# Performance work log

Measured on AMD Instinct MI355X. Metric: run time of the kernel, lower is better.

## Reference

```python
import jax, jax.numpy as jnp
import numpy as np

QMAX = 127.0  # 2**(8-1) - 1 for n_bits=8

def fake_quant_last_dim(t):
    # per-row absmax fake quant over last dim (per-token for acts, per-channel for weights)
    scales = jnp.max(jnp.abs(t), axis=-1, keepdims=True)
    scales = jnp.clip(scales, 1e-05, None) / QMAX
    return jnp.round(t / scales) * scales

def setup_inputs() -> dict:
    key = jax.random.key(0)
    k1, k2, k3 = jax.random.split(key, 3)
    B, S, D_in, D_out = 4, 2048, 4096, 4096
    return {
        "input": jax.random.normal(k1, (B, S, D_in), dtype=jnp.float32),
        "weight": jax.random.normal(k2, (D_out, D_in), dtype=jnp.float32) * 0.02,
        "bias": jax.random.normal(k3, (D_out,), dtype=jnp.float32) * 0.02,
    }

def reference(input, weight, bias):
    w_q = fake_quant_last_dim(weight)          # per-output-channel
    x_q = fake_quant_last_dim(input)           # per-token
    y = jnp.einsum('bsi,oi->bso', x_q, w_q) + bias
    return fake_quant_last_dim(y)              # per-token output quant
```

## Files before the change

### kernel.cpp

```cpp
#include <hip/hip_runtime.h>

typedef unsigned int u32;
typedef __attribute__((ext_vector_type(4))) int i32x4;

#define BM 256
#define BN 256
#define BKT 64

__device__ __forceinline__ void gload16(const void* g, void* l) {
  __builtin_amdgcn_global_load_lds(
      (const __attribute__((address_space(1))) unsigned int*)g,
      (__attribute__((address_space(3))) unsigned int*)l, 16, 0, 0);
}

__device__ __forceinline__ u32 pack4_i8(float4 v, float scale) {
  const int a = (int)rintf(v.x / scale);
  const int b = (int)rintf(v.y / scale);
  const int c = (int)rintf(v.z / scale);
  const int d = (int)rintf(v.w / scale);
  return (u32)(a & 255) | (((u32)(b & 255)) << 8) |
         (((u32)(c & 255)) << 16) | (((u32)(d & 255)) << 24);
}

__global__ __launch_bounds__(256) void quant_rows4096_kernel(
    const float* __restrict__ src, u32* __restrict__ q,
    float* __restrict__ scales)
{
  const size_t row = blockIdx.x;
  const float4* __restrict__ p = (const float4*)(src + row * 4096);
  const int t = threadIdx.x;
  float4 v0 = p[t];
  float4 v1 = p[t + 256];
  float4 v2 = p[t + 512];
  float4 v3 = p[t + 768];
  float m = 0.0f;
  m = fmaxf(m, fmaxf(fmaxf(fabsf(v0.x), fabsf(v0.y)), fmaxf(fabsf(v0.z), fabsf(v0.w))));
  m = fmaxf(m, fmaxf(fmaxf(fabsf(v1.x), fabsf(v1.y)), fmaxf(fabsf(v1.z), fabsf(v1.w))));
  m = fmaxf(m, fmaxf(fmaxf(fabsf(v2.x), fabsf(v2.y)), fmaxf(fabsf(v2.z), fabsf(v2.w))));
  m = fmaxf(m, fmaxf(fmaxf(fabsf(v3.x), fabsf(v3.y)), fmaxf(fabsf(v3.z), fabsf(v3.w))));
  #pragma unroll
  for (int off = 32; off > 0; off >>= 1) m = fmaxf(m, __shfl_xor(m, off));
  __shared__ float wmax[4];
  if ((t & 63) == 0) wmax[t >> 6] = m;
  __syncthreads();
  m = fmaxf(fmaxf(wmax[0], wmax[1]), fmaxf(wmax[2], wmax[3]));
  const float scale = fmaxf(m, 1e-5f) * (1.0f / 127.0f);
  if (t == 0) scales[row] = scale;
  u32* __restrict__ qp = q + row * 1024;
  qp[t]       = pack4_i8(v0, scale);
  qp[t + 256] = pack4_i8(v1, scale);
  qp[t + 512] = pack4_i8(v2, scale);
  qp[t + 768] = pack4_i8(v3, scale);
}

__global__ __launch_bounds__(256) void quant_rows_kernel(
    const float* __restrict__ src, u32* __restrict__ q,
    float* __restrict__ scales, int K)
{
  const size_t row = blockIdx.x;
  const float* __restrict__ p = src + row * (size_t)K;
  const int t = threadIdx.x;
  const int nv = K >> 2;
  float m = 0.0f;
  for (int i = t; i < nv; i += 256) {
    float4 v = ((const float4*)p)[i];
    m = fmaxf(m, fmaxf(fmaxf(fabsf(v.x), fabsf(v.y)),
                       fmaxf(fabsf(v.z), fabsf(v.w))));
  }
  #pragma unroll
  for (int off = 32; off > 0; off >>= 1) m = fmaxf(m, __shfl_xor(m, off));
  __shared__ float wmax[4];
  if ((t & 63) == 0) wmax[t >> 6] = m;
  __syncthreads();
  m = fmaxf(fmaxf(wmax[0], wmax[1]), fmaxf(wmax[2], wmax[3]));
  const float scale = fmaxf(m, 1e-5f) * (1.0f / 127.0f);
  if (t == 0) scales[row] = scale;
  u32* __restrict__ qp = q + row * ((size_t)K >> 2);
  for (int i = t; i < nv; i += 256) {
    float4 v = ((const float4*)p)[i];
    qp[i] = pack4_i8(v, scale);
  }
}

__global__ __launch_bounds__(512, 2) void gemm_bt_kernel(
    const signed char* __restrict__ Aq, const signed char* __restrict__ Bq,
    const float* __restrict__ sx, const float* __restrict__ sw,
    const float* __restrict__ bias, float* __restrict__ Y,
    unsigned int* __restrict__ rowmax, int M, int N, int K)
{
  __shared__ signed char lds[4][2][BM * 64];

  int bid = (int)blockIdx.x;
  const int nwg = (int)gridDim.x;
  if ((nwg & 7) == 0) {
    const int cpx = nwg >> 3;
    bid = (bid & 7) * cpx + (bid >> 3);
  }
  const int ntile = N / BN;
  const size_t brow = (size_t)(bid / ntile) * BM;
  const size_t bcol = (size_t)(bid % ntile) * BN;

  const int t = threadIdx.x;
  const int lane = t & 63;
  const int wid = t >> 6;
  const int wr = wid >> 2, wc = wid & 3;
  const int g4 = lane >> 4, l16 = lane & 15;

  const int parity = l16 & 1;
  const int w8 = (l16 >> 1) & 7;
  const int sp = (g4 + (parity << 2)) ^ w8;
  const int abase = (wr * 64 + (l16 >> 1)) * 128 + sp * 16;
  const int bbase = (wc * 32 + (l16 >> 1)) * 128 + sp * 16;

  const int q0 = (t & 7) ^ ((t >> 3) & 7);
  const int srow = 2 * (t >> 3) + (q0 >> 2);
  const int scol = (q0 & 3) * 16;
  const signed char* srcA = Aq + (brow + srow) * (size_t)K + scol;
  const signed char* srcB = Bq + (bcol + srow) * (size_t)K + scol;
  const int dstb = t * 16;

  i32x4 acc0[4][4] = {};
  i32x4 acc1[4][4] = {};
  const int nK = K / BKT;

  i32x4 aA0, aA1, aA2, aA3;
  i32x4 aC0, aC1, aC2, aC3;
  i32x4 bA0, bA1, bA2, bA3;

#define STAGE4(S, TT) do { \
    gload16(srcA + (size_t)(TT) * 64,                      &lds[S][0][dstb]); \
    gload16(srcA + 128 * (size_t)K + (size_t)(TT) * 64,    &lds[S][0][8192 + dstb]); \
    gload16(srcB + (size_t)(TT) * 64,                      &lds[S][1][dstb]); \
    gload16(srcB + 128 * (size_t)K + (size_t)(TT) * 64,    &lds[S][1][8192 + dstb]); \
  } while (0)
#define BARS() do { asm volatile("" ::: "memory"); \
                    __builtin_amdgcn_s_barrier(); \
                    asm volatile("" ::: "memory"); } while (0)
#define VMWS(NN) asm volatile("s_waitcnt vmcnt(" #NN ")" ::: "memory")
#define RDA(P, S, MH) do { \
    P##0 = *(const i32x4*)&lds[S][0][abase + (MH) * 4096 +    0]; \
    P##1 = *(const i32x4*)&lds[S][0][abase + (MH) * 4096 + 1024]; \
    P##2 = *(const i32x4*)&lds[S][0][abase + (MH) * 4096 + 2048]; \
    P##3 = *(const i32x4*)&lds[S][0][abase + (MH) * 4096 + 3072]; } while (0)
#define RDB(P, S) do { \
    P##0 = *(const i32x4*)&lds[S][1][bbase +    0]; \
    P##1 = *(const i32x4*)&lds[S][1][bbase + 1024]; \
    P##2 = *(const i32x4*)&lds[S][1][bbase + 2048]; \
    P##3 = *(const i32x4*)&lds[S][1][bbase + 3072]; } while (0)
#define MF(ACC, A, B) do { \
    ACC[0][0] = __builtin_amdgcn_mfma_i32_16x16x64_i8(A##0, B##0, ACC[0][0], 0, 0, 0); \
    ACC[0][1] = __builtin_amdgcn_mfma_i32_16x16x64_i8(A##0, B##1, ACC[0][1], 0, 0, 0); \
    ACC[0][2] = __builtin_amdgcn_mfma_i32_16x16x64_i8(A##0, B##2, ACC[0][2], 0, 0, 0); \
    ACC[0][3] = __builtin_amdgcn_mfma_i32_16x16x64_i8(A##0, B##3, ACC[0][3], 0, 0, 0); \
    ACC[1][0] = __builtin_amdgcn_mfma_i32_16x16x64_i8(A##1, B##0, ACC[1][0], 0, 0, 0); \
    ACC[1][1] = __builtin_amdgcn_mfma_i32_16x16x64_i8(A##1, B##1, ACC[1][1], 0, 0, 0); \
    ACC[1][2] = __builtin_amdgcn_mfma_i32_16x16x64_i8(A##1, B##2, ACC[1][2], 0, 0, 0); \
    ACC[1][3] = __builtin_amdgcn_mfma_i32_16x16x64_i8(A##1, B##3, ACC[1][3], 0, 0, 0); \
    ACC[2][0] = __builtin_amdgcn_mfma_i32_16x16x64_i8(A##2, B##0, ACC[2][0], 0, 0, 0); \
    ACC[2][1] = __builtin_amdgcn_mfma_i32_16x16x64_i8(A##2, B##1, ACC[2][1], 0, 0, 0); \
    ACC[2][2] = __builtin_amdgcn_mfma_i32_16x16x64_i8(A##2, B##2, ACC[2][2], 0, 0, 0); \
    ACC[2][3] = __builtin_amdgcn_mfma_i32_16x16x64_i8(A##2, B##3, ACC[2][3], 0, 0, 0); \
    ACC[3][0] = __builtin_amdgcn_mfma_i32_16x16x64_i8(A##3, B##0, ACC[3][0], 0, 0, 0); \
    ACC[3][1] = __builtin_amdgcn_mfma_i32_16x16x64_i8(A##3, B##1, ACC[3][1], 0, 0, 0); \
    ACC[3][2] = __builtin_amdgcn_mfma_i32_16x16x64_i8(A##3, B##2, ACC[3][2], 0, 0, 0); \
    ACC[3][3] = __builtin_amdgcn_mfma_i32_16x16x64_i8(A##3, B##3, ACC[3][3], 0, 0, 0); } while (0)

#define WIN_ST(S, TT) do { \
    VMWS(8); \
    BARS(); \
    STAGE4((S + 3) & 3, TT); \
    RDA(aA, S, 0); \
    RDB(bA, S); \
    __builtin_amdgcn_s_setprio(1); \
    MF(acc0, aA, bA); \
    __builtin_amdgcn_s_setprio(0); \
    RDA(aC, S, 1); \
    __builtin_amdgcn_s_setprio(1); \
    MF(acc1, aC, bA); \
    __builtin_amdgcn_s_setprio(0); \
  } while (0)
#define WIN_NS(S, VN) do { \
    VMWS(VN); \
    BARS(); \
    RDA(aA, S, 0); \
    RDB(bA, S); \
    __builtin_amdgcn_s_setprio(1); \
    MF(acc0, aA, bA); \
    __builtin_amdgcn_s_setprio(0); \
    RDA(aC, S, 1); \
    __builtin_amdgcn_s_setprio(1); \
    MF(acc1, aC, bA); \
    __builtin_amdgcn_s_setprio(0); \
  } while (0)

  STAGE4(0, 0);
  STAGE4(1, 1);
  STAGE4(2, 2);

  int kt = 0;
  for (; kt + 8 <= nK; kt += 4) {
    WIN_ST(0, kt + 3);
    WIN_ST(1, kt + 4);
    WIN_ST(2, kt + 5);
    WIN_ST(3, kt + 6);
  }
  WIN_ST(0, nK - 1);
  WIN_NS(1, 8);
  WIN_NS(2, 4);
  WIN_NS(3, 0);

  float swv[4], biv[4];
  size_t gcolv[4];
  #pragma unroll
  for (int j = 0; j < 4; ++j) {
    gcolv[j] = bcol + wc * 64 + j * 16 + l16;
    swv[j] = sw[gcolv[j]];
    biv[j] = bias[gcolv[j]];
  }
  #pragma unroll
  for (int mh = 0; mh < 2; ++mh) {
    #pragma unroll
    for (int i = 0; i < 4; ++i) {
      #pragma unroll
      for (int r = 0; r < 4; ++r) {
        const size_t grow = brow + (size_t)(wr * 128 + mh * 64 + i * 16 + g4 * 4 + r);
        const float sxr = sx[grow];
        float* yrow = Y + grow * (size_t)N;
        float rmax = 0.0f;
        #pragma unroll
        for (int j = 0; j < 4; ++j) {
          const int av = mh ? acc1[i][j][r] : acc0[i][j][r];
          const float y = (float)av * (sxr * swv[j]) + biv[j];
          yrow[gcolv[j]] = y;
          rmax = fmaxf(rmax, fabsf(y));
        }
        rmax = fmaxf(rmax, __shfl_xor(rmax, 1));
        rmax = fmaxf(rmax, __shfl_xor(rmax, 2));
        rmax = fmaxf(rmax, __shfl_xor(rmax, 4));
        rmax = fmaxf(rmax, __shfl_xor(rmax, 8));
        if (l16 == 0)
          atomicMax(&rowmax[grow], __float_as_uint(rmax));
      }
    }
  }
#undef STAGE4
#undef BARS
#undef VMWS
#undef RDA
#undef RDB
#undef MF
#undef WIN_ST
#undef WIN_NS
}

__global__ __launch_bounds__(256) void outquant_kernel(
    float* __restrict__ Y, const unsigned int* __restrict__ rowmax, int N)
{
  const size_t row = blockIdx.x;
  const float amax = __uint_as_float(rowmax[row]);
  const float scale = fmaxf(amax, 1e-5f) * (1.0f / 127.0f);
  float* __restrict__ p = Y + row * (size_t)N;
  const int nv = N >> 2;
  for (int i = threadIdx.x; i < nv; i += 256) {
    float4 v = ((float4*)p)[i];
    v.x = rintf(v.x / scale) * scale;
    v.y = rintf(v.y / scale) * scale;
    v.z = rintf(v.z / scale) * scale;
    v.w = rintf(v.w / scale) * scale;
    ((float4*)p)[i] = v;
  }
}

extern "C" void kernel_launch(void* const* d_in, const int* in_sizes, int n_in,
                              void* d_out, int out_size, void* d_ws, size_t ws_size,
                              hipStream_t stream)
{
  const float* x = (const float*)d_in[0];
  const float* wgt = (const float*)d_in[1];
  const float* bias = (const float*)d_in[2];
  float* out = (float*)d_out;

  const int N = in_sizes[2];
  const int K = in_sizes[1] / N;
  const int M = in_sizes[0] / K;

  char* ws = (char*)d_ws;
  signed char* qx = (signed char*)ws;  ws += (size_t)M * K;
  signed char* qw = (signed char*)ws;  ws += (size_t)N * K;
  float* sx = (float*)ws;              ws += (size_t)M * sizeof(float);
  float* sw = (float*)ws;              ws += (size_t)N * sizeof(float);
  unsigned int* rowmax = (unsigned int*)ws;

  hipMemsetAsync(rowmax, 0, (size_t)M * sizeof(unsigned int), stream);

  if (K == 4096) {
    quant_rows4096_kernel<<<M, 256, 0, stream>>>(x, (u32*)qx, sx);
    quant_rows4096_kernel<<<N, 256, 0, stream>>>(wgt, (u32*)qw, sw);
  } else {
    quant_rows_kernel<<<M, 256, 0, stream>>>(x, (u32*)qx, sx, K);
    quant_rows_kernel<<<N, 256, 0, stream>>>(wgt, (u32*)qw, sw, K);
  }

  const int grid = (M / BM) * (N / BN);
  gemm_bt_kernel<<<grid, 512, 0, stream>>>(qx, qw, sx, sw, bias, out, rowmax, M, N, K);

  outquant_kernel<<<M, 256, 0, stream>>>(out, rowmax, N);
}
```

Before: 250.9 us.

## Switch int8 GEMM from 16x16x64 to 32x32x32 MFMA tiles

Replaces the 16x16x64 i8 MFMA inner loop with 32x32x32 i8 MFMA, reorganizing each wave's accumulators into 4x2 tiles of 16-wide vectors. LDS fragment addressing is redone for the 32-row lane layout, and each k-tile is split into two 32-deep halves. The epilogue is remapped to the new accumulator layout, widening the row-max shuffle reduction to 32 lanes. The aim is fewer MFMA issues and fewer LDS fragment reads per FLOP. The risk is changed LDS bank-conflict behavior, different register pressure, and longer per-instruction latency.

```diff
diff --git a/kernel.cpp b/kernel.cpp
--- a/kernel.cpp
+++ b/kernel.cpp
@@ -2,6 +2,7 @@
 
 typedef unsigned int u32;
 typedef __attribute__((ext_vector_type(4))) int i32x4;
+typedef __attribute__((ext_vector_type(16))) int i32x16;
 
 #define BM 256
 #define BN 256
@@ -104,13 +105,18 @@
   const int lane = t & 63;
   const int wid = t >> 6;
   const int wr = wid >> 2, wc = wid & 3;
-  const int g4 = lane >> 4, l16 = lane & 15;
-
-  const int parity = l16 & 1;
-  const int w8 = (l16 >> 1) & 7;
-  const int sp = (g4 + (parity << 2)) ^ w8;
-  const int abase = (wr * 64 + (l16 >> 1)) * 128 + sp * 16;
-  const int bbase = (wc * 32 + (l16 >> 1)) * 128 + sp * 16;
+  const int l31 = lane & 31;
+  const int l5 = lane >> 5;
+  const int parity = lane & 1;
+
+  const int aoff = l5 + (parity << 2);
+  const int amask = (l31 >> 1) & 7;
+  const int arp = wr * 64 + (l31 >> 1);
+  const int brp = wc * 32 + (l31 >> 1);
+  const int abase0 = arp * 128 + (((aoff + 0) ^ amask) << 4);
+  const int abase1 = arp * 128 + (((aoff + 2) ^ amask) << 4);
+  const int bbase0 = brp * 128 + (((aoff + 0) ^ amask) << 4);
+  const int bbase1 = brp * 128 + (((aoff + 2) ^ amask) << 4);
 
   const int q0 = (t & 7) ^ ((t >> 3) & 7);
   const int srow = 2 * (t >> 3) + (q0 >> 2);
@@ -119,13 +125,11 @@
   const signed char* srcB = Bq + (bcol + srow) * (size_t)K + scol;
   const int dstb = t * 16;
 
-  i32x4 acc0[4][4] = {};
-  i32x4 acc1[4][4] = {};
+  i32x16 acc[4][2] = {};
   const int nK = K / BKT;
 
-  i32x4 aA0, aA1, aA2, aA3;
-  i32x4 aC0, aC1, aC2, aC3;
-  i32x4 bA0, bA1, bA2, bA3;
+  i32x4 fa0, fa1, fa2, fa3;
+  i32x4 fb0, fb1;
 
 #define STAGE4(S, TT) do { \
     gload16(srcA + (size_t)(TT) * 64,                      &lds[S][0][dstb]); \
@@ -137,60 +141,41 @@
                     __builtin_amdgcn_s_barrier(); \
                     asm volatile("" ::: "memory"); } while (0)
 #define VMWS(NN) asm volatile("s_waitcnt vmcnt(" #NN ")" ::: "memory")
-#define RDA(P, S, MH) do { \
-    P##0 = *(const i32x4*)&lds[S][0][abase + (MH) * 4096 +    0]; \
-    P##1 = *(const i32x4*)&lds[S][0][abase + (MH) * 4096 + 1024]; \
-    P##2 = *(const i32x4*)&lds[S][0][abase + (MH) * 4096 + 2048]; \
-    P##3 = *(const i32x4*)&lds[S][0][abase + (MH) * 4096 + 3072]; } while (0)
-#define RDB(P, S) do { \
-    P##0 = *(const i32x4*)&lds[S][1][bbase +    0]; \
-    P##1 = *(const i32x4*)&lds[S][1][bbase + 1024]; \
-    P##2 = *(const i32x4*)&lds[S][1][bbase + 2048]; \
-    P##3 = *(const i32x4*)&lds[S][1][bbase + 3072]; } while (0)
-#define MF(ACC, A, B) do { \
-    ACC[0][0] = __builtin_amdgcn_mfma_i32_16x16x64_i8(A##0, B##0, ACC[0][0], 0, 0, 0); \
-    ACC[0][1] = __builtin_amdgcn_mfma_i32_16x16x64_i8(A##0, B##1, ACC[0][1], 0, 0, 0); \
-    ACC[0][2] = __builtin_amdgcn_mfma_i32_16x16x64_i8(A##0, B##2, ACC[0][2], 0, 0, 0); \
-    ACC[0][3] = __builtin_amdgcn_mfma_i32_16x16x64_i8(A##0, B##3, ACC[0][3], 0, 0, 0); \
-    ACC[1][0] = __builtin_amdgcn_mfma_i32_16x16x64_i8(A##1, B##0, ACC[1][0], 0, 0, 0); \
-    ACC[1][1] = __builtin_amdgcn_mfma_i32_16x16x64_i8(A##1, B##1, ACC[1][1], 0, 0, 0); \
-    ACC[1][2] = __builtin_amdgcn_mfma_i32_16x16x64_i8(A##1, B##2, ACC[1][2], 0, 0, 0); \
-    ACC[1][3] = __builtin_amdgcn_mfma_i32_16x16x64_i8(A##1, B##3, ACC[1][3], 0, 0, 0); \
-    ACC[2][0] = __builtin_amdgcn_mfma_i32_16x16x64_i8(A##2, B##0, ACC[2][0], 0, 0, 0); \
-    ACC[2][1] = __builtin_amdgcn_mfma_i32_16x16x64_i8(A##2, B##1, ACC[2][1], 0, 0, 0); \
-    ACC[2][2] = __builtin_amdgcn_mfma_i32_16x16x64_i8(A##2, B##2, ACC[2][2], 0, 0, 0); \
-    ACC[2][3] = __builtin_amdgcn_mfma_i32_16x16x64_i8(A##2, B##3, ACC[2][3], 0, 0, 0); \
-    ACC[3][0] = __builtin_amdgcn_mfma_i32_16x16x64_i8(A##3, B##0, ACC[3][0], 0, 0, 0); \
-    ACC[3][1] = __builtin_amdgcn_mfma_i32_16x16x64_i8(A##3, B##1, ACC[3][1], 0, 0, 0); \
-    ACC[3][2] = __builtin_amdgcn_mfma_i32_16x16x64_i8(A##3, B##2, ACC[3][2], 0, 0, 0); \
-    ACC[3][3] = __builtin_amdgcn_mfma_i32_16x16x64_i8(A##3, B##3, ACC[3][3], 0, 0, 0); } while (0)
+#define RDAB(S, AB) do { \
+    fa0 = *(const i32x4*)&lds[S][0][AB##a +    0]; \
+    fa1 = *(const i32x4*)&lds[S][0][AB##a + 2048]; \
+    fa2 = *(const i32x4*)&lds[S][0][AB##a + 4096]; \
+    fa3 = *(const i32x4*)&lds[S][0][AB##a + 6144]; \
+    fb0 = *(const i32x4*)&lds[S][1][AB##b +    0]; \
+    fb1 = *(const i32x4*)&lds[S][1][AB##b + 2048]; } while (0)
+  const int k0a = abase0, k0b = bbase0, k1a = abase1, k1b = bbase1;
+#define MF8() do { \
+    acc[0][0] = __builtin_amdgcn_mfma_i32_32x32x32_i8(fa0, fb0, acc[0][0], 0, 0, 0); \
+    acc[0][1] = __builtin_amdgcn_mfma_i32_32x32x32_i8(fa0, fb1, acc[0][1], 0, 0, 0); \
+    acc[1][0] = __builtin_amdgcn_mfma_i32_32x32x32_i8(fa1, fb0, acc[1][0], 0, 0, 0); \
+    acc[1][1] = __builtin_amdgcn_mfma_i32_32x32x32_i8(fa1, fb1, acc[1][1], 0, 0, 0); \
+    acc[2][0] = __builtin_amdgcn_mfma_i32_32x32x32_i8(fa2, fb0, acc[2][0], 0, 0, 0); \
+    acc[2][1] = __builtin_amdgcn_mfma_i32_32x32x32_i8(fa2, fb1, acc[2][1], 0, 0, 0); \
+    acc[3][0] = __builtin_amdgcn_mfma_i32_32x32x32_i8(fa3, fb0, acc[3][0], 0, 0, 0); \
+    acc[3][1] = __builtin_amdgcn_mfma_i32_32x32x32_i8(fa3, fb1, acc[3][1], 0, 0, 0); \
+  } while (0)
 
 #define WIN_ST(S, TT) do { \
     VMWS(8); \
     BARS(); \
     STAGE4((S + 3) & 3, TT); \
-    RDA(aA, S, 0); \
-    RDB(bA, S); \
-    __builtin_amdgcn_s_setprio(1); \
-    MF(acc0, aA, bA); \
-    __builtin_amdgcn_s_setprio(0); \
-    RDA(aC, S, 1); \
-    __builtin_amdgcn_s_setprio(1); \
-    MF(acc1, aC, bA); \
-    __builtin_amdgcn_s_setprio(0); \
+    RDAB(S, k0); \
+    __builtin_amdgcn_s_setprio(1); MF8(); __builtin_amdgcn_s_setprio(0); \
+    RDAB(S, k1); \
+    __builtin_amdgcn_s_setprio(1); MF8(); __builtin_amdgcn_s_setprio(0); \
   } while (0)
 #define WIN_NS(S, VN) do { \
     VMWS(VN); \
     BARS(); \
-    RDA(aA, S, 0); \
-    RDB(bA, S); \
-    __builtin_amdgcn_s_setprio(1); \
-    MF(acc0, aA, bA); \
-    __builtin_amdgcn_s_setprio(0); \
-    RDA(aC, S, 1); \
-    __builtin_amdgcn_s_setprio(1); \
-    MF(acc1, aC, bA); \
-    __builtin_amdgcn_s_setprio(0); \
+    RDAB(S, k0); \
+    __builtin_amdgcn_s_setprio(1); MF8(); __builtin_amdgcn_s_setprio(0); \
+    RDAB(S, k1); \
+    __builtin_amdgcn_s_setprio(1); MF8(); __builtin_amdgcn_s_setprio(0); \
   } while (0)
 
   STAGE4(0, 0);
@@ -209,46 +194,43 @@
   WIN_NS(2, 4);
   WIN_NS(3, 0);
 
-  float swv[4], biv[4];
-  size_t gcolv[4];
-  #pragma unroll
-  for (int j = 0; j < 4; ++j) {
-    gcolv[j] = bcol + wc * 64 + j * 16 + l16;
-    swv[j] = sw[gcolv[j]];
-    biv[j] = bias[gcolv[j]];
-  }
-  #pragma unroll
-  for (int mh = 0; mh < 2; ++mh) {
+  float swv[2], biv[2];
+  size_t gcolv[2];
+  #pragma unroll
+  for (int nj = 0; nj < 2; ++nj) {
+    gcolv[nj] = bcol + wc * 64 + nj * 32 + l31;
+    swv[nj] = sw[gcolv[nj]];
+    biv[nj] = bias[gcolv[nj]];
+  }
+  #pragma unroll
+  for (int mi = 0; mi < 4; ++mi) {
     #pragma unroll
-    for (int i = 0; i < 4; ++i) {
+    for (int reg = 0; reg < 16; ++reg) {
+      const size_t grow = brow + (size_t)(wr * 128 + mi * 32 +
+                                          (reg & 3) + 8 * (reg >> 2) + 4 * l5);
+      const float sxr = sx[grow];
+      float* yrow = Y + grow * (size_t)N;
+      float rmax = 0.0f;
       #pragma unroll
-      for (int r = 0; r < 4; ++r) {
-        const size_t grow = brow + (size_t)(wr * 128 + mh * 64 + i * 16 + g4 * 4 + r);
-        const float sxr = sx[grow];
-        float* yrow = Y + grow * (size_t)N;
-        float rmax = 0.0f;
-        #pragma unroll
-        for (int j = 0; j < 4; ++j) {
-          const int av = mh ? acc1[i][j][r] : acc0[i][j][r];
-          const float y = (float)av * (sxr * swv[j]) + biv[j];
-          yrow[gcolv[j]] = y;
-          rmax = fmaxf(rmax, fabsf(y));
-        }
-        rmax = fmaxf(rmax, __shfl_xor(rmax, 1));
-        rmax = fmaxf(rmax, __shfl_xor(rmax, 2));
-        rmax = fmaxf(rmax, __shfl_xor(rmax, 4));
-        rmax = fmaxf(rmax, __shfl_xor(rmax, 8));
-        if (l16 == 0)
-          atomicMax(&rowmax[grow], __float_as_uint(rmax));
+      for (int nj = 0; nj < 2; ++nj) {
+        const float y = (float)acc[mi][nj][reg] * (sxr * swv[nj]) + biv[nj];
+        yrow[gcolv[nj]] = y;
+        rmax = fmaxf(rmax, fabsf(y));
       }
+      rmax = fmaxf(rmax, __shfl_xor(rmax, 1));
+      rmax = fmaxf(rmax, __shfl_xor(rmax, 2));
+      rmax = fmaxf(rmax, __shfl_xor(rmax, 4));
+      rmax = fmaxf(rmax, __shfl_xor(rmax, 8));
+      rmax = fmaxf(rmax, __shfl_xor(rmax, 16));
+      if (l31 == 0)
+        atomicMax(&rowmax[grow], __float_as_uint(rmax));
     }
   }
 #undef STAGE4
 #undef BARS
 #undef VMWS
-#undef RDA
-#undef RDB
-#undef MF
+#undef RDAB
+#undef MF8
 #undef WIN_ST
 #undef WIN_NS
 }
```

Result: slower. 311.9 us (+24.3%).

## Reorder GEMM k-loop so LDS reads precede the wait and barrier

Applied to the files above, without the earlier changes.

The main-loop window now issues the next global-to-LDS stage and all LDS fragment reads for the current slot first. Only then does it wait on outstanding vector memory and hit the barrier, and it runs both MFMA groups back to back under raised priority. The first wait and barrier move ahead of the loop, so each barrier now guards readiness of the next slot rather than the current one. The aim is to hide LDS read latency and barrier stalls behind in-flight loads. The cost is higher register pressure, since all A/B fragments are live at once, and a more fragile synchronisation protocol.

```diff
diff --git a/kernel.cpp b/kernel.cpp
--- a/kernel.cpp
+++ b/kernel.cpp
@@ -165,50 +165,38 @@
     ACC[3][2] = __builtin_amdgcn_mfma_i32_16x16x64_i8(A##3, B##2, ACC[3][2], 0, 0, 0); \
     ACC[3][3] = __builtin_amdgcn_mfma_i32_16x16x64_i8(A##3, B##3, ACC[3][3], 0, 0, 0); } while (0)
 
-#define WIN_ST(S, TT) do { \
-    VMWS(8); \
-    BARS(); \
-    STAGE4((S + 3) & 3, TT); \
+#define WIN(S, ST, TT, HASVM, VN) do { \
+    if (ST) STAGE4((S + 3) & 3, TT); \
     RDA(aA, S, 0); \
     RDB(bA, S); \
+    RDA(aC, S, 1); \
+    if (HASVM) { VMWS(VN); } \
+    BARS(); \
     __builtin_amdgcn_s_setprio(1); \
     MF(acc0, aA, bA); \
-    __builtin_amdgcn_s_setprio(0); \
-    RDA(aC, S, 1); \
-    __builtin_amdgcn_s_setprio(1); \
     MF(acc1, aC, bA); \
     __builtin_amdgcn_s_setprio(0); \
   } while (0)
-#define WIN_NS(S, VN) do { \
-    VMWS(VN); \
-    BARS(); \
-    RDA(aA, S, 0); \
-    RDB(bA, S); \
-    __builtin_amdgcn_s_setprio(1); \
-    MF(acc0, aA, bA); \
-    __builtin_amdgcn_s_setprio(0); \
-    RDA(aC, S, 1); \
-    __builtin_amdgcn_s_setprio(1); \
-    MF(acc1, aC, bA); \
-    __builtin_amdgcn_s_setprio(0); \
-  } while (0)
 
   STAGE4(0, 0);
   STAGE4(1, 1);
   STAGE4(2, 2);
+  VMWS(8);
+  BARS();
 
   int kt = 0;
   for (; kt + 8 <= nK; kt += 4) {
-    WIN_ST(0, kt + 3);
-    WIN_ST(1, kt + 4);
-    WIN_ST(2, kt + 5);
-    WIN_ST(3, kt + 6);
-  }
-  WIN_ST(0, nK - 1);
-  WIN_NS(1, 8);
-  WIN_NS(2, 4);
-  WIN_NS(3, 0);
-
+    WIN(0, 1, kt + 3, 1, 8);
+    WIN(1, 1, kt + 4, 1, 8);
+    WIN(2, 1, kt + 5, 1, 8);
+    WIN(3, 1, kt + 6, 1, 8);
+  }
+  WIN(0, 1, nK - 1, 1, 8);
+  WIN(1, 0, 0, 1, 4);
+  WIN(2, 0, 0, 1, 0);
+  WIN(3, 0, 0, 0, 0);
+
+  const int g4e = g4;
   float swv[4], biv[4];
   size_t gcolv[4];
   #pragma unroll
@@ -223,7 +211,7 @@
     for (int i = 0; i < 4; ++i) {
       #pragma unroll
       for (int r = 0; r < 4; ++r) {
-        const size_t grow = brow + (size_t)(wr * 128 + mh * 64 + i * 16 + g4 * 4 + r);
+        const size_t grow = brow + (size_t)(wr * 128 + mh * 64 + i * 16 + g4e * 4 + r);
         const float sxr = sx[grow];
         float* yrow = Y + grow * (size_t)N;
         float rmax = 0.0f;
@@ -249,8 +237,7 @@
 #undef RDA
 #undef RDB
 #undef MF
-#undef WIN_ST
-#undef WIN_NS
+#undef WIN
 }
 
 __global__ __launch_bounds__(256) void outquant_kernel(
```

New measurement: 246.7 us. No clear change (-1.7%).
